# Performance work log

Hardware: AMD Instinct MI355X
Metric: run time of the kernel (lower is better)

The kernel has to match this reference:

```python
import jax, jax.numpy as jnp
import numpy as np

N_NODES = 50000
N_EDGES = 800000
D_IN = 128
D_OUT = 128


def setup_inputs() -> dict:
    key = jax.random.key(0)
    k1, k2, k3, k4, k5 = jax.random.split(key, 5)
    H = jax.random.normal(k1, (N_NODES, D_IN), dtype=jnp.float32)
    stdv = 1.0 / np.sqrt(D_OUT)
    W = jax.random.uniform(k2, (D_IN, D_OUT), dtype=jnp.float32, minval=-stdv, maxval=stdv)
    bias = jnp.zeros((D_OUT,), dtype=jnp.float32)
    edge_vals = jax.random.uniform(k3, (N_EDGES,), dtype=jnp.float32)
    edge_rows = jax.random.randint(k4, (N_EDGES,), 0, N_NODES, dtype=jnp.int32)
    edge_cols = jax.random.randint(k5, (N_EDGES,), 0, N_NODES, dtype=jnp.int32)
    return {"H": H, "W": W, "bias": bias, "edge_vals": edge_vals,
            "edge_rows": edge_rows, "edge_cols": edge_cols}


def reference(H, W, bias, edge_vals, edge_rows, edge_cols):
    # H' = relu(A @ (H W) + b), A given as COO edge list (rows, cols, vals)
    n = H.shape[0]
    HW = H @ W  # [N, D_out]
    # SpMM: out[r] = sum_{e: row(e)=r} val(e) * HW[col(e)]
    msgs = edge_vals[:, None] * HW[edge_cols]  # [E, D_out]
    out = jax.ops.segment_sum(msgs, edge_rows, num_segments=n)
    out = out + bias
    return jax.nn.relu(out)
```

## Files before the change

### kernel.cpp

```cpp
#include <hip/hip_runtime.h>

#define D 128
#define BM 64
#define NBS 256
#define BINSH 6
#define MAXBINS 1024
#define CAPB 1536
#define EBUF 3200

typedef __attribute__((ext_vector_type(8))) short bf16x8;
typedef __attribute__((ext_vector_type(4))) float f32x4;

__device__ __forceinline__ unsigned short f2bf(float f) {
    unsigned u = __float_as_uint(f);
    u = (u + 0x7FFFu + ((u >> 16) & 1u)) >> 16;
    return (unsigned short)u;
}
__device__ __forceinline__ float bf2f(unsigned short h) {
    return __uint_as_float(((unsigned)h) << 16);
}

__global__ __launch_bounds__(128) void k_prepw(const float* __restrict__ W,
                                               unsigned short* __restrict__ Wt) {
    int nn = blockIdx.x, k = threadIdx.x;
    Wt[nn * D + k] = f2bf(W[k * D + nn]);
}

__global__ __launch_bounds__(256) void k_gemm(const float* __restrict__ H,
                                              const unsigned short* __restrict__ Wt,
                                              unsigned short* __restrict__ HWb,
                                              int n) {
    __shared__ unsigned short sA[BM * 64];
    __shared__ unsigned short sB[D * 64];
    const int tid = threadIdx.x;
    const int row0 = blockIdx.x * BM;
    const int w = tid >> 6, l = tid & 63;
    const int lr = l & 15, lq = l >> 4;

    f32x4 acc[8];
#pragma unroll
    for (int ct = 0; ct < 8; ++ct) acc[ct] = (f32x4){0.f, 0.f, 0.f, 0.f};

#pragma unroll
    for (int kt = 0; kt < 2; ++kt) {
        if (kt) __syncthreads();
#pragma unroll
        for (int s = 0; s < 4; ++s) {
            int idx = s * 256 + tid;
            int r = idx >> 3, cc = idx & 7;
            bf16x8 v = *reinterpret_cast<const bf16x8*>(&Wt[(size_t)r * D + kt * 64 + cc * 8]);
            *reinterpret_cast<bf16x8*>(&sB[r * 64 + ((cc ^ (r & 7)) * 8)]) = v;
        }
#pragma unroll
        for (int s = 0; s < 2; ++s) {
            int idx = s * 256 + tid;
            int r = idx >> 3, cc = idx & 7;
            int row = row0 + r;
            float4 u0 = make_float4(0.f, 0.f, 0.f, 0.f), u1 = u0;
            if (row < n) {
                const float4* p = reinterpret_cast<const float4*>(
                    &H[(size_t)row * D + kt * 64 + cc * 8]);
                u0 = p[0]; u1 = p[1];
            }
            bf16x8 v;
            v[0] = (short)f2bf(u0.x); v[1] = (short)f2bf(u0.y);
            v[2] = (short)f2bf(u0.z); v[3] = (short)f2bf(u0.w);
            v[4] = (short)f2bf(u1.x); v[5] = (short)f2bf(u1.y);
            v[6] = (short)f2bf(u1.z); v[7] = (short)f2bf(u1.w);
            *reinterpret_cast<bf16x8*>(&sA[r * 64 + ((cc ^ (r & 7)) * 8)]) = v;
        }
        __syncthreads();

#pragma unroll
        for (int ks = 0; ks < 2; ++ks) {
            const int arow = w * 16 + lr;
            const int acc_c = (ks * 4 + lq) ^ (arow & 7);
            bf16x8 a = *reinterpret_cast<const bf16x8*>(&sA[arow * 64 + acc_c * 8]);
#pragma unroll
            for (int ct = 0; ct < 8; ++ct) {
                const int brow = ct * 16 + lr;
                const int bcc = (ks * 4 + lq) ^ (brow & 7);
                bf16x8 b = *reinterpret_cast<const bf16x8*>(&sB[brow * 64 + bcc * 8]);
                acc[ct] = __builtin_amdgcn_mfma_f32_16x16x32_bf16(b, a, acc[ct], 0, 0, 0);
            }
        }
    }

    int row = row0 + w * 16 + lr;
    if (row < n) {
#pragma unroll
        for (int ct = 0; ct < 8; ++ct) {
            ushort4 o;
            o.x = f2bf(acc[ct][0]); o.y = f2bf(acc[ct][1]);
            o.z = f2bf(acc[ct][2]); o.w = f2bf(acc[ct][3]);
            *reinterpret_cast<ushort4*>(&HWb[(size_t)row * D + ct * 16 + lq * 4]) = o;
        }
    }
}

__global__ __launch_bounds__(256) void k_bsort(const int* __restrict__ rows,
                                               const int* __restrict__ cols,
                                               const float* __restrict__ vals,
                                               int2* __restrict__ segs,
                                               int* __restrict__ offtT,
                                               int E, int nbins, int chunk) {
    __shared__ int hist[MAXBINS];
    __shared__ int excl[MAXBINS + 1];
    __shared__ int wsum[4];
    __shared__ int2 ebuf[EBUF];
    const int tid = threadIdx.x;
    const int p = blockIdx.x;
    const int s = p * chunk;
    int epos = s + chunk; if (epos > E) epos = E;
    const int len = (epos > s) ? (epos - s) : 0;

    for (int i = tid; i < nbins; i += 256) hist[i] = 0;
    __syncthreads();
    if (len > 0) {
        const int t0 = s + (len & ~3);
        for (int base = s + tid * 4; base + 4 <= epos; base += 1024) {
            int4 r4 = *reinterpret_cast<const int4*>(&rows[base]);
            atomicAdd(&hist[r4.x >> BINSH], 1);
            atomicAdd(&hist[r4.y >> BINSH], 1);
            atomicAdd(&hist[r4.z >> BINSH], 1);
            atomicAdd(&hist[r4.w >> BINSH], 1);
        }
        for (int e = t0 + tid; e < epos; e += 256)
            atomicAdd(&hist[rows[e] >> BINSH], 1);
    }
    __syncthreads();

    int b0 = tid * 4;
    int h0 = 0, h1 = 0, h2 = 0, h3 = 0, sum = 0;
    if (b0 < nbins) {
        h0 = hist[b0];
        h1 = (b0 + 1 < nbins) ? hist[b0 + 1] : 0;
        h2 = (b0 + 2 < nbins) ? hist[b0 + 2] : 0;
        h3 = (b0 + 3 < nbins) ? hist[b0 + 3] : 0;
        sum = h0 + h1 + h2 + h3;
    }
    {
        int lane = tid & 63, w = tid >> 6;
        int inc = sum;
#pragma unroll
        for (int o = 1; o < 64; o <<= 1) {
            int t = __shfl_up(inc, o);
            if (lane >= o) inc += t;
        }
        if (lane == 63) wsum[w] = inc;
        __syncthreads();
        int wex = 0;
        for (int j = 0; j < w; ++j) wex += wsum[j];
        int cur = wex + inc - sum;
        if (b0 < nbins) {
            excl[b0] = cur; hist[b0] = cur; cur += h0;
            if (b0 + 1 < nbins) { excl[b0 + 1] = cur; hist[b0 + 1] = cur; cur += h1; }
            if (b0 + 2 < nbins) { excl[b0 + 2] = cur; hist[b0 + 2] = cur; cur += h2; }
            if (b0 + 3 < nbins) { excl[b0 + 3] = cur; hist[b0 + 3] = cur; cur += h3; }
        }
        if (tid == 255) excl[nbins] = len;
    }
    __syncthreads();

    if (len > 0) {
        const int t0 = s + (len & ~3);
        for (int base = s + tid * 4; base + 4 <= epos; base += 1024) {
            int4 r4 = *reinterpret_cast<const int4*>(&rows[base]);
            int4 c4 = *reinterpret_cast<const int4*>(&cols[base]);
            float4 v4 = *reinterpret_cast<const float4*>(&vals[base]);
            int q0 = atomicAdd(&hist[r4.x >> BINSH], 1);
            int q1 = atomicAdd(&hist[r4.y >> BINSH], 1);
            int q2 = atomicAdd(&hist[r4.z >> BINSH], 1);
            int q3 = atomicAdd(&hist[r4.w >> BINSH], 1);
            ebuf[q0] = make_int2(((r4.x & 63) << 16) | c4.x, __float_as_int(v4.x));
            ebuf[q1] = make_int2(((r4.y & 63) << 16) | c4.y, __float_as_int(v4.y));
            ebuf[q2] = make_int2(((r4.z & 63) << 16) | c4.z, __float_as_int(v4.z));
            ebuf[q3] = make_int2(((r4.w & 63) << 16) | c4.w, __float_as_int(v4.w));
        }
        for (int e = t0 + tid; e < epos; e += 256) {
            int r = rows[e];
            int q = atomicAdd(&hist[r >> BINSH], 1);
            ebuf[q] = make_int2(((r & 63) << 16) | cols[e], __float_as_int(vals[e]));
        }
    }
    __syncthreads();

    for (int i = tid; i < len; i += 256)
        segs[(size_t)p * chunk + i] = ebuf[i];
    for (int i = tid; i <= nbins; i += 256)
        offtT[(size_t)i * NBS + p] = p * chunk + excl[i];
}

__global__ __launch_bounds__(512) void k_spmm(const unsigned short* __restrict__ HWb,
                                              const int* __restrict__ offtT,
                                              const int2* __restrict__ segs,
                                              const float* __restrict__ bias,
                                              float* __restrict__ out, int n, int nbins) {
    __shared__ int2 ent[CAPB];
    __shared__ int2 sent[CAPB];
    __shared__ int lcnt[64];
    __shared__ int loff[64];
    __shared__ int lcur[64];
    __shared__ int wsum[8];
    __shared__ int total_s;
    const int b = blockIdx.x;
    const int tid = threadIdx.x;

    int o0 = 0, c = 0;
    if (tid < NBS) {
        o0 = offtT[(size_t)b * NBS + tid];
        int o1 = offtT[(size_t)(b + 1) * NBS + tid];
        c = o1 - o0;
    }
    {
        int lane = tid & 63, w = tid >> 6;
        int inc = c;
#pragma unroll
        for (int o = 1; o < 64; o <<= 1) {
            int t = __shfl_up(inc, o);
            if (lane >= o) inc += t;
        }
        if (lane == 63) wsum[w] = inc;
        __syncthreads();
        int wex = 0;
        for (int j = 0; j < w; ++j) wex += wsum[j];
        int myoff = wex + inc - c;
        if (tid == 511) total_s = wex + inc;
        for (int j = 0; j < c; ++j) {
            int q = myoff + j;
            if (q < CAPB) ent[q] = segs[o0 + j];
        }
    }
    if (tid < 64) lcnt[tid] = 0;
    __syncthreads();
    int cnt = total_s;
    if (cnt > CAPB) cnt = CAPB;

    for (int i = tid; i < cnt; i += 512)
        atomicAdd(&lcnt[((unsigned)ent[i].x) >> 16], 1);
    __syncthreads();
    if (tid < 64) {
        int v = lcnt[tid];
        int inc = v;
#pragma unroll
        for (int o = 1; o < 64; o <<= 1) {
            int t = __shfl_up(inc, o);
            if (tid >= o) inc += t;
        }
        loff[tid] = inc - v;
        lcur[tid] = inc - v;
    }
    __syncthreads();
    for (int i = tid; i < cnt; i += 512) {
        int2 e = ent[i];
        int q = atomicAdd(&lcur[((unsigned)e.x) >> 16], 1);
        sent[q] = e;
    }
    __syncthreads();

    const int w = tid >> 6, lane = tid & 63;
    const unsigned c2 = 2 * lane;
    const float2 bb = *reinterpret_cast<const float2*>(&bias[c2]);

    for (int rr = w; rr < 64; rr += 8) {
        int row = b * 64 + rr;
        if (row >= n) break;
        int s = loff[rr];
        int deg = lcnt[rr];
        float a0 = 0.f, a1 = 0.f, b0 = 0.f, b1 = 0.f;
        int t = 0;
        for (; t + 8 <= deg; t += 8) {
            int2 e0 = sent[s + t],     e1 = sent[s + t + 1];
            int2 e2 = sent[s + t + 2], e3 = sent[s + t + 3];
            int2 e4 = sent[s + t + 4], e5 = sent[s + t + 5];
            int2 e6 = sent[s + t + 6], e7 = sent[s + t + 7];
            unsigned m0 = *reinterpret_cast<const unsigned*>(&HWb[(size_t)(e0.x & 0xFFFF) * D + c2]);
            unsigned m1 = *reinterpret_cast<const unsigned*>(&HWb[(size_t)(e1.x & 0xFFFF) * D + c2]);
            unsigned m2 = *reinterpret_cast<const unsigned*>(&HWb[(size_t)(e2.x & 0xFFFF) * D + c2]);
            unsigned m3 = *reinterpret_cast<const unsigned*>(&HWb[(size_t)(e3.x & 0xFFFF) * D + c2]);
            unsigned m4 = *reinterpret_cast<const unsigned*>(&HWb[(size_t)(e4.x & 0xFFFF) * D + c2]);
            unsigned m5 = *reinterpret_cast<const unsigned*>(&HWb[(size_t)(e5.x & 0xFFFF) * D + c2]);
            unsigned m6 = *reinterpret_cast<const unsigned*>(&HWb[(size_t)(e6.x & 0xFFFF) * D + c2]);
            unsigned m7 = *reinterpret_cast<const unsigned*>(&HWb[(size_t)(e7.x & 0xFFFF) * D + c2]);
            float v0 = __int_as_float(e0.y), v1 = __int_as_float(e1.y);
            float v2 = __int_as_float(e2.y), v3 = __int_as_float(e3.y);
            float v4 = __int_as_float(e4.y), v5 = __int_as_float(e5.y);
            float v6 = __int_as_float(e6.y), v7 = __int_as_float(e7.y);
            a0 += v0 * bf2f((unsigned short)(m0 & 0xFFFF));
            a1 += v0 * bf2f((unsigned short)(m0 >> 16));
            b0 += v1 * bf2f((unsigned short)(m1 & 0xFFFF));
            b1 += v1 * bf2f((unsigned short)(m1 >> 16));
            a0 += v2 * bf2f((unsigned short)(m2 & 0xFFFF));
            a1 += v2 * bf2f((unsigned short)(m2 >> 16));
            b0 += v3 * bf2f((unsigned short)(m3 & 0xFFFF));
            b1 += v3 * bf2f((unsigned short)(m3 >> 16));
            a0 += v4 * bf2f((unsigned short)(m4 & 0xFFFF));
            a1 += v4 * bf2f((unsigned short)(m4 >> 16));
            b0 += v5 * bf2f((unsigned short)(m5 & 0xFFFF));
            b1 += v5 * bf2f((unsigned short)(m5 >> 16));
            a0 += v6 * bf2f((unsigned short)(m6 & 0xFFFF));
            a1 += v6 * bf2f((unsigned short)(m6 >> 16));
            b0 += v7 * bf2f((unsigned short)(m7 & 0xFFFF));
            b1 += v7 * bf2f((unsigned short)(m7 >> 16));
        }
        for (; t < deg; ++t) {
            int2 e = sent[s + t];
            unsigned m = *reinterpret_cast<const unsigned*>(&HWb[(size_t)(e.x & 0xFFFF) * D + c2]);
            float v = __int_as_float(e.y);
            a0 += v * bf2f((unsigned short)(m & 0xFFFF));
            a1 += v * bf2f((unsigned short)(m >> 16));
        }
        float2 o;
        o.x = fmaxf(a0 + b0 + bb.x, 0.f);
        o.y = fmaxf(a1 + b1 + bb.y, 0.f);
        *reinterpret_cast<float2*>(&out[(size_t)row * D + c2]) = o;
    }
}

__global__ void k_init_bias(const float* __restrict__ bias, float* __restrict__ out, int n) {
    int i = blockIdx.x * blockDim.x + threadIdx.x;
    if (i < n * D) out[i] = bias[i & (D - 1)];
}
__global__ void k_scatter(const unsigned short* __restrict__ HWb, const int* __restrict__ rows,
                          const int* __restrict__ cols, const float* __restrict__ vals,
                          float* __restrict__ out, int E) {
    int e = blockIdx.x * 2 + (threadIdx.x >> 7);
    int j = threadIdx.x & (D - 1);
    if (e < E) {
        int r = rows[e];
        int c = cols[e];
        float v = vals[e];
        atomicAdd(&out[(size_t)r * D + j], v * bf2f(HWb[(size_t)c * D + j]));
    }
}
__global__ void k_relu(float* __restrict__ out, int n) {
    int i = blockIdx.x * blockDim.x + threadIdx.x;
    if (i < n * D) out[i] = fmaxf(out[i], 0.f);
}

extern "C" void kernel_launch(void* const* d_in, const int* in_sizes, int n_in,
                              void* d_out, int out_size, void* d_ws, size_t ws_size,
                              hipStream_t stream) {
    const float* H         = (const float*)d_in[0];
    const float* W         = (const float*)d_in[1];
    const float* bias      = (const float*)d_in[2];
    const float* edge_vals = (const float*)d_in[3];
    const int*   edge_rows = (const int*)d_in[4];
    const int*   edge_cols = (const int*)d_in[5];
    float* out = (float*)d_out;

    const int n = in_sizes[0] / D;
    const int E = in_sizes[3];
    const int gblocks = (n + BM - 1) / BM;
    const int nbins = (n + 63) >> BINSH;
    int chunk = (E + NBS - 1) / NBS;
    chunk = (chunk + 3) & ~3;

    char* ws = (char*)d_ws;
    unsigned short* HWb = (unsigned short*)ws; ws += (size_t)n * D * sizeof(unsigned short);
    unsigned short* Wt  = (unsigned short*)ws; ws += (size_t)D * D * sizeof(unsigned short);
    int2* segs = (int2*)ws;          ws += (size_t)NBS * chunk * sizeof(int2);
    int* offtT = (int*)ws;           ws += (size_t)(nbins + 1) * NBS * sizeof(int);
    size_t need_full = (size_t)(ws - (char*)d_ws);

    k_prepw<<<D, D, 0, stream>>>(W, Wt);
    k_gemm<<<gblocks, 256, 0, stream>>>(H, Wt, HWb, n);

    if (ws_size >= need_full && n < 65536 && nbins <= MAXBINS && chunk <= EBUF) {
        k_bsort<<<NBS, 256, 0, stream>>>(edge_rows, edge_cols, edge_vals,
                                         segs, offtT, E, nbins, chunk);
        k_spmm<<<nbins, 512, 0, stream>>>(HWb, offtT, segs, bias, out, n, nbins);
    } else {
        k_init_bias<<<((size_t)n * D + 255) / 256, 256, 0, stream>>>(bias, out, n);
        k_scatter<<<(E + 1) / 2, 256, 0, stream>>>(HWb, edge_rows, edge_cols, edge_vals, out, E);
        k_relu<<<((size_t)n * D + 255) / 256, 256, 0, stream>>>(out, n);
    }
}
```

Before: 70.33 us.

## Merge GEMM and edge bucket-sort into one launch with block-index dispatch

Fuses the dense H·W GEMM kernel and the COO bucket-sort kernel into a single launch. Blocks below gblocks do the GEMM and the rest do the sort, with the two shared-memory layouts overlaid in a union. The two independent stages can then run concurrently on the GPU, and one launch plus the inter-kernel gap goes away. In exchange, the shared-memory footprint per block is now the larger of the two (the sort's ~33KB), which can lower GEMM occupancy.

```diff
diff --git a/kernel.cpp b/kernel.cpp
--- a/kernel.cpp
+++ b/kernel.cpp
@@ -26,90 +26,98 @@
     Wt[nn * D + k] = f2bf(W[k * D + nn]);
 }
 
-__global__ __launch_bounds__(256) void k_gemm(const float* __restrict__ H,
-                                              const unsigned short* __restrict__ Wt,
-                                              unsigned short* __restrict__ HWb,
-                                              int n) {
-    __shared__ unsigned short sA[BM * 64];
-    __shared__ unsigned short sB[D * 64];
+__global__ __launch_bounds__(256) void k_gemm_bsort(const float* __restrict__ H,
+                                                    const unsigned short* __restrict__ Wt,
+                                                    unsigned short* __restrict__ HWb,
+                                                    int n,
+                                                    const int* __restrict__ rows,
+                                                    const int* __restrict__ cols,
+                                                    const float* __restrict__ vals,
+                                                    int2* __restrict__ segs,
+                                                    int* __restrict__ offtT,
+                                                    int E, int nbins, int chunk,
+                                                    int gblocks) {
+    __shared__ union {
+        struct { unsigned short sA[BM * 64]; unsigned short sB[D * 64]; } g;
+        struct { int hist[MAXBINS]; int excl[MAXBINS + 1]; int wsum[4];
+                 int2 ebuf[EBUF]; } s;
+    } u;
     const int tid = threadIdx.x;
-    const int row0 = blockIdx.x * BM;
-    const int w = tid >> 6, l = tid & 63;
-    const int lr = l & 15, lq = l >> 4;
-
-    f32x4 acc[8];
-#pragma unroll
-    for (int ct = 0; ct < 8; ++ct) acc[ct] = (f32x4){0.f, 0.f, 0.f, 0.f};
-
-#pragma unroll
-    for (int kt = 0; kt < 2; ++kt) {
-        if (kt) __syncthreads();
-#pragma unroll
-        for (int s = 0; s < 4; ++s) {
-            int idx = s * 256 + tid;
-            int r = idx >> 3, cc = idx & 7;
-            bf16x8 v = *reinterpret_cast<const bf16x8*>(&Wt[(size_t)r * D + kt * 64 + cc * 8]);
-            *reinterpret_cast<bf16x8*>(&sB[r * 64 + ((cc ^ (r & 7)) * 8)]) = v;
-        }
-#pragma unroll
-        for (int s = 0; s < 2; ++s) {
-            int idx = s * 256 + tid;
-            int r = idx >> 3, cc = idx & 7;
-            int row = row0 + r;
-            float4 u0 = make_float4(0.f, 0.f, 0.f, 0.f), u1 = u0;
-            if (row < n) {
-                const float4* p = reinterpret_cast<const float4*>(
-                    &H[(size_t)row * D + kt * 64 + cc * 8]);
-                u0 = p[0]; u1 = p[1];
+
+    if (blockIdx.x < (unsigned)gblocks) {
+        unsigned short* sA = u.g.sA;
+        unsigned short* sB = u.g.sB;
+        const int row0 = blockIdx.x * BM;
+        const int w = tid >> 6, l = tid & 63;
+        const int lr = l & 15, lq = l >> 4;
+
+        f32x4 acc[8];
+#pragma unroll
+        for (int ct = 0; ct < 8; ++ct) acc[ct] = (f32x4){0.f, 0.f, 0.f, 0.f};
+
+#pragma unroll
+        for (int kt = 0; kt < 2; ++kt) {
+            if (kt) __syncthreads();
+#pragma unroll
+            for (int s = 0; s < 4; ++s) {
+                int idx = s * 256 + tid;
+                int r = idx >> 3, cc = idx & 7;
+                bf16x8 v = *reinterpret_cast<const bf16x8*>(&Wt[(size_t)r * D + kt * 64 + cc * 8]);
+                *reinterpret_cast<bf16x8*>(&sB[r * 64 + ((cc ^ (r & 7)) * 8)]) = v;
             }
-            bf16x8 v;
-            v[0] = (short)f2bf(u0.x); v[1] = (short)f2bf(u0.y);
-            v[2] = (short)f2bf(u0.z); v[3] = (short)f2bf(u0.w);
-            v[4] = (short)f2bf(u1.x); v[5] = (short)f2bf(u1.y);
-            v[6] = (short)f2bf(u1.z); v[7] = (short)f2bf(u1.w);
-            *reinterpret_cast<bf16x8*>(&sA[r * 64 + ((cc ^ (r & 7)) * 8)]) = v;
-        }
-        __syncthreads();
-
-#pragma unroll
-        for (int ks = 0; ks < 2; ++ks) {
-            const int arow = w * 16 + lr;
-            const int acc_c = (ks * 4 + lq) ^ (arow & 7);
-            bf16x8 a = *reinterpret_cast<const bf16x8*>(&sA[arow * 64 + acc_c * 8]);
+#pragma unroll
+            for (int s = 0; s < 2; ++s) {
+                int idx = s * 256 + tid;
+                int r = idx >> 3, cc = idx & 7;
+                int row = row0 + r;
+                float4 u0 = make_float4(0.f, 0.f, 0.f, 0.f), u1 = u0;
+                if (row < n) {
+                    const float4* p = reinterpret_cast<const float4*>(
+                        &H[(size_t)row * D + kt * 64 + cc * 8]);
+                    u0 = p[0]; u1 = p[1];
+                }
+                bf16x8 v;
+                v[0] = (short)f2bf(u0.x); v[1] = (short)f2bf(u0.y);
+                v[2] = (short)f2bf(u0.z); v[3] = (short)f2bf(u0.w);
+                v[4] = (short)f2bf(u1.x); v[5] = (short)f2bf(u1.y);
+                v[6] = (short)f2bf(u1.z); v[7] = (short)f2bf(u1.w);
+                *reinterpret_cast<bf16x8*>(&sA[r * 64 + ((cc ^ (r & 7)) * 8)]) = v;
+            }
+            __syncthreads();
+
+#pragma unroll
+            for (int ks = 0; ks < 2; ++ks) {
+                const int arow = w * 16 + lr;
+                const int acc_c = (ks * 4 + lq) ^ (arow & 7);
+                bf16x8 a = *reinterpret_cast<const bf16x8*>(&sA[arow * 64 + acc_c * 8]);
+#pragma unroll
+                for (int ct = 0; ct < 8; ++ct) {
+                    const int brow = ct * 16 + lr;
+                    const int bcc = (ks * 4 + lq) ^ (brow & 7);
+                    bf16x8 b = *reinterpret_cast<const bf16x8*>(&sB[brow * 64 + bcc * 8]);
+                    acc[ct] = __builtin_amdgcn_mfma_f32_16x16x32_bf16(b, a, acc[ct], 0, 0, 0);
+                }
+            }
+        }
+
+        int row = row0 + w * 16 + lr;
+        if (row < n) {
 #pragma unroll
             for (int ct = 0; ct < 8; ++ct) {
-                const int brow = ct * 16 + lr;
-                const int bcc = (ks * 4 + lq) ^ (brow & 7);
-                bf16x8 b = *reinterpret_cast<const bf16x8*>(&sB[brow * 64 + bcc * 8]);
-                acc[ct] = __builtin_amdgcn_mfma_f32_16x16x32_bf16(b, a, acc[ct], 0, 0, 0);
+                ushort4 o;
+                o.x = f2bf(acc[ct][0]); o.y = f2bf(acc[ct][1]);
+                o.z = f2bf(acc[ct][2]); o.w = f2bf(acc[ct][3]);
+                *reinterpret_cast<ushort4*>(&HWb[(size_t)row * D + ct * 16 + lq * 4]) = o;
             }
         }
-    }
-
-    int row = row0 + w * 16 + lr;
-    if (row < n) {
-#pragma unroll
-        for (int ct = 0; ct < 8; ++ct) {
-            ushort4 o;
-            o.x = f2bf(acc[ct][0]); o.y = f2bf(acc[ct][1]);
-            o.z = f2bf(acc[ct][2]); o.w = f2bf(acc[ct][3]);
-            *reinterpret_cast<ushort4*>(&HWb[(size_t)row * D + ct * 16 + lq * 4]) = o;
-        }
-    }
-}
-
-__global__ __launch_bounds__(256) void k_bsort(const int* __restrict__ rows,
-                                               const int* __restrict__ cols,
-                                               const float* __restrict__ vals,
-                                               int2* __restrict__ segs,
-                                               int* __restrict__ offtT,
-                                               int E, int nbins, int chunk) {
-    __shared__ int hist[MAXBINS];
-    __shared__ int excl[MAXBINS + 1];
-    __shared__ int wsum[4];
-    __shared__ int2 ebuf[EBUF];
-    const int tid = threadIdx.x;
-    const int p = blockIdx.x;
+        return;
+    }
+
+    int* hist = u.s.hist;
+    int* excl = u.s.excl;
+    int* wsum = u.s.wsum;
+    int2* ebuf = u.s.ebuf;
+    const int p = blockIdx.x - gblocks;
     const int s = p * chunk;
     int epos = s + chunk; if (epos > E) epos = E;
     const int len = (epos > s) ? (epos - s) : 0;
@@ -364,13 +372,16 @@
     size_t need_full = (size_t)(ws - (char*)d_ws);
 
     k_prepw<<<D, D, 0, stream>>>(W, Wt);
-    k_gemm<<<gblocks, 256, 0, stream>>>(H, Wt, HWb, n);
 
     if (ws_size >= need_full && n < 65536 && nbins <= MAXBINS && chunk <= EBUF) {
-        k_bsort<<<NBS, 256, 0, stream>>>(edge_rows, edge_cols, edge_vals,
-                                         segs, offtT, E, nbins, chunk);
+        k_gemm_bsort<<<gblocks + NBS, 256, 0, stream>>>(H, Wt, HWb, n,
+                                                        edge_rows, edge_cols, edge_vals,
+                                                        segs, offtT, E, nbins, chunk, gblocks);
         k_spmm<<<nbins, 512, 0, stream>>>(HWb, offtT, segs, bias, out, n, nbins);
     } else {
+        k_gemm_bsort<<<gblocks, 256, 0, stream>>>(H, Wt, HWb, n,
+                                                  edge_rows, edge_cols, edge_vals,
+                                                  (int2*)d_ws, (int*)d_ws, 0, nbins, chunk, gblocks);
         k_init_bias<<<((size_t)n * D + 255) / 256, 256, 0, stream>>>(bias, out, n);
         k_scatter<<<(E + 1) / 2, 256, 0, stream>>>(HWb, edge_rows, edge_cols, edge_vals, out, E);
         k_relu<<<((size_t)n * D + 255) / 256, 256, 0, stream>>>(out, n);
```

Result: faster. 65.06 us (-7.5%).
